# Kernel optimization log

Measured on AMD Instinct MI355X. Metric: run time of the kernel, lower is better.

## Reference

```python
import jax, jax.numpy as jnp
import numpy as np

H, W = 128, 192          # image size (height, width) after imsz swap
K = 31                   # weight_sl (local window size)
T = K // 2               # replicate padding
C_FEAT = 64              # feat_dim
FFT_ROWS, FFT_COLS = 32, 48  # rect fft mask (after '48,32' swap)


def fft_rect(x):
    # rfft2 low-pass rectangular mask, exactly as fft_ifft with 'rect'.
    f = jnp.fft.rfft2(x)
    rows = jnp.arange(f.shape[-2])[:, None] < FFT_ROWS
    cols = jnp.arange(f.shape[-1])[None, :] < FFT_COLS
    f = f * (rows & cols)
    return jnp.fft.irfft2(f, s=x.shape[-2:])


def make_grid():
    t = float(T)  # weight_sl//2 with downsample_factor=1
    xs = jnp.linspace(-t, t, K)
    gx, gy = jnp.meshgrid(xs, xs, indexing='ij')
    return jnp.stack((gx, gy), axis=-1)  # [K,K,2]


def local_corr(src, tgt):
    # src, tgt: [C,H,W] -> cost volume [H,W,K,K]
    sp = jnp.pad(src, ((0, 0), (T, T), (T, T)), mode='edge')  # replicate pad
    rows = []
    for k in range(K):  # fixed structural loop over window rows
        sl = sp[:, k:k + H, :]  # [C,H,W+2T]
        win = jax.lax.conv_general_dilated_patches(sl[None], (1, K), (1, 1), 'VALID')[0]
        win = win.reshape(C_FEAT, K, H, W)  # [C,l,H,W]
        rows.append(jnp.einsum('chw,clhw->hwl', tgt, win))
    return jnp.stack(rows, axis=-2)  # [H,W,k,l]


def setup_inputs() -> dict:
    key = jax.random.key(0)
    k1, k2, k3 = jax.random.split(key, 3)
    fill_val = (1.0 / C_FEAT) ** 0.5
    feats = fill_val + 0.02 * jax.random.normal(k1, (1, 2, C_FEAT, H, W), jnp.float32)
    in_frames = jax.random.normal(k2, (1, 1, 3, H, W), jnp.float32)
    tgt_frames = jax.random.normal(k3, (1, 1, 3, H, W), jnp.float32)
    return {"in_frames": in_frames, "tgt_frames": tgt_frames, "feats": feats, "temp": 10}


def reference(in_frames, tgt_frames, feats, temp):
    # src_idx=0, tgt_idx=1, single-frame 'feats' path
    src = fft_rect(feats[0, 0])  # [C,H,W]
    tgt = fft_rect(feats[0, 1])
    # bilinear interpolate(scale_factor=1) is identity
    src = src / jnp.linalg.norm(src, axis=0, keepdims=True)
    tgt = tgt / jnp.linalg.norm(tgt, axis=0, keepdims=True)
    w = local_corr(src, tgt) * temp                       # [H,W,K,K]
    w = jax.nn.softmax(w.reshape(H, W, K * K), axis=-1).reshape(H, W, K, K)

    # windowed average of in_frames with per-pixel softmax weights
    xp = jnp.pad(in_frames[0, 0], ((0, 0), (T, T), (T, T)), mode='edge')
    patches = jax.lax.conv_general_dilated_patches(xp[None], (K, K), (1, 1), 'VALID')[0]
    patches = patches.reshape(3, K, K, H, W)              # [C,k,l,H,W]
    out = jnp.einsum('cklhw,hwkl->chw', patches, w)[None, None]  # [1,1,3,H,W]

    grid = make_grid()                                    # [K,K,2]
    pos = jnp.einsum('hwkl,klm->hwm', w, grid)[None, None]
    pos = pos[..., ::-1]                                  # .flip(-1)
    enorm = jnp.einsum('hwkl,kl->hw', w, jnp.linalg.norm(grid, axis=-1))[None, None]
    weights = w[None, None]                               # [1,1,H,W,K,K]
    return out, pos, enorm, weights
```

## Files before the change

### kernel.cpp

```cpp
#include <hip/hip_runtime.h>
#include <cstddef>

#define H 128
#define W 192
#define KS 31
#define CF 64
#define NPIX (H*W)
#define NKL (KS*KS)

#define OFF_POS (3*NPIX)
#define OFF_EN  (OFF_POS + 2*NPIX)
#define OFF_WGT (OFF_EN + NPIX)

#define NIMG NPIX
#define WS_CWT 0
#define WS_SWT 512
#define WS_CHT 1024
#define WS_SHT 1536
#define WS_U   2048
#define WS_V   (WS_U + 128*NIMG)
#define WS_Y   (WS_V + 128*NIMG)
#define WS_SN  (WS_Y + 128*NIMG)
#define WS_TN  (WS_SN + 32*NIMG)

#define PI_F 3.14159265358979323846f

typedef __attribute__((ext_vector_type(8))) short short8v;
typedef __attribute__((ext_vector_type(4))) float f32x4;

__device__ inline ushort bf16rtn(float f){
  uint u = __float_as_uint(f);
  u += 0x7fffu + ((u >> 16) & 1u);
  return (ushort)(u >> 16);
}

__global__ __launch_bounds__(256) void k_tables(float* ws){
  int t = blockIdx.x*256 + threadIdx.x;
  if (t < 383){
    int d = t - 191;
    float c = 1.0f, s = 0.0f;
    for (int v = 1; v < 48; ++v){
      int m = (v*d) % 192; if (m < 0) m += 192;
      float a = (2.0f*PI_F/192.0f)*(float)m;
      c += 2.0f*cosf(a);
      s += 2.0f*sinf(a);
    }
    ws[WS_CWT + t] = c * (1.0f/192.0f);
    ws[WS_SWT + t] = s * (1.0f/192.0f);
  } else if (t < 383 + 255){
    int i = t - 383;
    int d = i - 127;
    float c = 0.0f, s = 0.0f;
    for (int u = 0; u < 32; ++u){
      int m = (u*d) % 128; if (m < 0) m += 128;
      float a = (2.0f*PI_F/128.0f)*(float)m;
      c += cosf(a);
      s += sinf(a);
    }
    ws[WS_CHT + i] = c * (1.0f/128.0f);
    ws[WS_SHT + i] = s * (1.0f/128.0f);
  }
}

__global__ __launch_bounds__(192) void k_colpass(const float* __restrict__ feats,
                                                const float* __restrict__ ws,
                                                float* __restrict__ U,
                                                float* __restrict__ V){
  __shared__ float xs[8][192];
  int w  = threadIdx.x;
  int R0 = blockIdx.x * 8;
  for (int r = 0; r < 8; ++r) xs[r][w] = feats[(size_t)(R0 + r)*192 + w];
  __syncthreads();
  const float* cwt = ws + WS_CWT;
  const float* swt = ws + WS_SWT;
  float u[8], v[8];
#pragma unroll
  for (int r = 0; r < 8; ++r){ u[r] = 0.0f; v[r] = 0.0f; }
  for (int wp = 0; wp < 192; ++wp){
    float cw = cwt[w - wp + 191];
    float sw = swt[w - wp + 191];
#pragma unroll
    for (int r = 0; r < 8; ++r){
      float x = xs[r][wp];
      u[r] = fmaf(x, cw, u[r]);
      v[r] = fmaf(x, sw, v[r]);
    }
  }
  for (int r = 0; r < 8; ++r){
    U[(size_t)(R0 + r)*192 + w] = u[r];
    V[(size_t)(R0 + r)*192 + w] = v[r];
  }
}

__global__ __launch_bounds__(192) void k_rowpass(const float* __restrict__ U,
                                                const float* __restrict__ V,
                                                const float* __restrict__ ws,
                                                float* __restrict__ Y){
  __shared__ float scht[255], ssht[255];
  int w = threadIdx.x;
  for (int i = w; i < 255; i += 192){
    scht[i] = ws[WS_CHT + i];
    ssht[i] = ws[WS_SHT + i];
  }
  __syncthreads();
  int ch = blockIdx.x >> 3;
  int h0 = (blockIdx.x & 7) * 16;
  const float* Uc = U + (size_t)ch*NIMG;
  const float* Vc = V + (size_t)ch*NIMG;
  float acc[16];
#pragma unroll
  for (int r = 0; r < 16; ++r) acc[r] = 0.0f;
  for (int hp = 0; hp < 128; ++hp){
    float uu = Uc[hp*192 + w];
    float vv = Vc[hp*192 + w];
#pragma unroll
    for (int r = 0; r < 16; ++r){
      int idx = h0 + r - hp + 127;
      acc[r] = fmaf(uu,  scht[idx], acc[r]);
      acc[r] = fmaf(-vv, ssht[idx], acc[r]);
    }
  }
  for (int r = 0; r < 16; ++r)
    Y[(size_t)ch*NIMG + (h0 + r)*192 + w] = acc[r];
}

__global__ __launch_bounds__(192) void k_norm(const float* __restrict__ Y,
                                              ushort* __restrict__ SNh,
                                              ushort* __restrict__ TNh){
  int h = blockIdx.x, w = threadIdx.x;
  int which = blockIdx.y;
  int pix = h*192 + w;
  const float* base = Y + (size_t)which*64*NIMG + pix;
  float x[64];
  float ss = 0.0f;
#pragma unroll
  for (int c = 0; c < 64; ++c){
    x[c] = base[(size_t)c*NIMG];
    ss = fmaf(x[c], x[c], ss);
  }
  float rn = 1.0f / sqrtf(ss);
  ushort* o = (which ? TNh : SNh) + (size_t)pix*64;
#pragma unroll
  for (int q = 0; q < 8; ++q){
    ushort tmp[8];
#pragma unroll
    for (int e = 0; e < 8; ++e) tmp[e] = bf16rtn(x[q*8 + e] * rn);
    *reinterpret_cast<uint4*>(o + q*8) = *reinterpret_cast<const uint4*>(tmp);
  }
}

__global__ __launch_bounds__(256) void k_corr(const ushort* __restrict__ SNh,
                                              const ushort* __restrict__ TNh,
                                              const int* __restrict__ temp,
                                              float* __restrict__ wgt){
  int h = blockIdx.x, k = blockIdx.y;
  int lane = threadIdx.x & 63;
  int wv = threadIdx.x >> 6;
  int i0base = wv * 3;
  int n = lane & 15, g = lane >> 4;
  float tempf = (float)(*temp);
  int sh = h + k - 15; sh = sh < 0 ? 0 : (sh > 127 ? 127 : sh);

  short8v a[3][2];
#pragma unroll
  for (int i = 0; i < 3; ++i){
    const ushort* p = TNh + ((size_t)(h*192 + (i0base + i)*16 + n))*64 + g*8;
#pragma unroll
    for (int ks = 0; ks < 2; ++ks)
      a[i][ks] = *reinterpret_cast<const short8v*>(p + ks*32);
  }
  short8v b[5][2];
  int j0lo = i0base - 1;
#pragma unroll
  for (int j = 0; j < 5; ++j){
    int j0 = j0lo + j;
    if (j0 < 0 || j0 > 11) continue;
    const ushort* p = SNh + ((size_t)(sh*192 + j0*16 + n))*64 + g*8;
#pragma unroll
    for (int ks = 0; ks < 2; ++ks)
      b[j][ks] = *reinterpret_cast<const short8v*>(p + ks*32);
  }

  float* base = wgt + ((size_t)(h*192))*NKL + (size_t)k*KS;
#pragma unroll
  for (int i = 0; i < 3; ++i){
    int i0 = i0base + i;
#pragma unroll
    for (int dj = -1; dj <= 1; ++dj){
      int j0 = i0 + dj;
      if (j0 < 0 || j0 > 11) continue;
      int jj = i + dj + 1;
      f32x4 acc = {0.0f, 0.0f, 0.0f, 0.0f};
      acc = __builtin_amdgcn_mfma_f32_16x16x32_bf16(a[i][0], b[jj][0], acc, 0, 0, 0);
      acc = __builtin_amdgcn_mfma_f32_16x16x32_bf16(a[i][1], b[jj][1], acc, 0, 0, 0);
      int sx = j0*16 + n;
#pragma unroll
      for (int r = 0; r < 4; ++r){
        int m = g*4 + r;
        int w = i0*16 + m;
        int l = sx - w + 15;
        float v = acc[r] * tempf;
        if (l >= 0 && l <= 30) base[(size_t)w*NKL + l] = v;
        if (j0 == 0 && n == 0){
          for (int l2 = 0; l2 < 15 - w; ++l2) base[(size_t)w*NKL + l2] = v;
        }
        if (j0 == 11 && n == 15){
          for (int l2 = 207 - w; l2 <= 30; ++l2) base[(size_t)w*NKL + l2] = v;
        }
      }
    }
  }
}

__global__ __launch_bounds__(256) void k_fused(float* __restrict__ dout,
                                               const float* __restrict__ frames){
  __shared__ float red[256];
  __shared__ float red6[6][256];
  int pix = blockIdx.x, t = threadIdx.x;
  int h = pix / 192, w = pix % 192;
  float* wp_ = dout + OFF_WGT + (size_t)pix*NKL;

  float x[4];
#pragma unroll
  for (int j = 0; j < 4; ++j){
    int i = t + 256*j;
    x[j] = (i < NKL) ? wp_[i] : -3.4e38f;
  }
  float m = fmaxf(fmaxf(x[0], x[1]), fmaxf(x[2], x[3]));
  red[t] = m; __syncthreads();
  for (int s = 128; s > 0; s >>= 1){
    if (t < s) red[t] = fmaxf(red[t], red[t + s]);
    __syncthreads();
  }
  float mall = red[0]; __syncthreads();

  float e[4];
  float sum = 0.0f;
#pragma unroll
  for (int j = 0; j < 4; ++j){
    int i = t + 256*j;
    e[j] = (i < NKL) ? expf(x[j] - mall) : 0.0f;
    sum += e[j];
  }
  red[t] = sum; __syncthreads();
  for (int s = 128; s > 0; s >>= 1){
    if (t < s) red[t] += red[t + s];
    __syncthreads();
  }
  float rs = 1.0f / red[0];

  float o0=0, o1=0, o2=0, p0=0, p1=0, en=0;
#pragma unroll
  for (int j = 0; j < 4; ++j){
    int i = t + 256*j;
    if (i < NKL){
      int k = i / 31, l = i - k*31;
      float ev = e[j] * rs;
      wp_[i] = ev;
      float dy = (float)(k - 15), dx = (float)(l - 15);
      p0 = fmaf(ev, dx, p0);
      p1 = fmaf(ev, dy, p1);
      en = fmaf(ev, sqrtf(dx*dx + dy*dy), en);
      int hh = h + k - 15; hh = hh < 0 ? 0 : (hh > 127 ? 127 : hh);
      int ww = w + l - 15; ww = ww < 0 ? 0 : (ww > 191 ? 191 : ww);
      const float* f = frames + hh*192 + ww;
      o0 = fmaf(ev, f[0],      o0);
      o1 = fmaf(ev, f[NPIX],   o1);
      o2 = fmaf(ev, f[2*NPIX], o2);
    }
  }
  red6[0][t]=o0; red6[1][t]=o1; red6[2][t]=o2; red6[3][t]=p0; red6[4][t]=p1; red6[5][t]=en;
  __syncthreads();
  for (int s = 128; s > 0; s >>= 1){
    if (t < s){
#pragma unroll
      for (int q = 0; q < 6; ++q) red6[q][t] += red6[q][t + s];
    }
    __syncthreads();
  }
  if (t == 0){
    dout[0*NPIX + pix] = red6[0][0];
    dout[1*NPIX + pix] = red6[1][0];
    dout[2*NPIX + pix] = red6[2][0];
    dout[OFF_POS + pix*2 + 0] = red6[3][0];
    dout[OFF_POS + pix*2 + 1] = red6[4][0];
    dout[OFF_EN + pix] = red6[5][0];
  }
}

extern "C" void kernel_launch(void* const* d_in, const int* in_sizes, int n_in,
                              void* d_out, int out_size, void* d_ws, size_t ws_size,
                              hipStream_t stream) {
  const float* frames = (const float*)d_in[0];
  const float* feats  = (const float*)d_in[2];
  const int*   temp   = (const int*)d_in[3];
  float* ws   = (float*)d_ws;
  float* dout = (float*)d_out;
  (void)in_sizes; (void)n_in; (void)out_size; (void)ws_size;

  float*  U   = ws + WS_U;
  float*  V   = ws + WS_V;
  float*  Y   = ws + WS_Y;
  ushort* SNh = (ushort*)(ws + WS_SN);
  ushort* TNh = (ushort*)(ws + WS_TN);

  hipLaunchKernelGGL(k_tables,  dim3(3),         dim3(256), 0, stream, ws);
  hipLaunchKernelGGL(k_colpass, dim3(2048),      dim3(192), 0, stream, feats, ws, U, V);
  hipLaunchKernelGGL(k_rowpass, dim3(1024),      dim3(192), 0, stream, U, V, ws, Y);
  hipLaunchKernelGGL(k_norm,    dim3(128, 2),    dim3(192), 0, stream, Y, SNh, TNh);
  hipLaunchKernelGGL(k_corr,    dim3(128, 31),   dim3(256), 0, stream, SNh, TNh, temp, dout + OFF_WGT);
  hipLaunchKernelGGL(k_fused,   dim3(NPIX),      dim3(256), 0, stream, dout, frames);
}
```

Baseline: 346.2 us.

## Fuse correlation, softmax and weighted reductions into one MFMA kernel

Merges the correlation kernel with the softmax/aggregation kernel. Each 64-thread block computes its correlation tiles with MFMA twice: the first pass accumulates the softmax sum and the weighted frame, position and norm sums in registers, and the second pass writes the normalized weights. The large cost volume is no longer written as raw logits and then read back, and the per-pixel 256-thread shared-memory reductions go away. The softmax max is fixed at temp (normalized features bound the dot product by 1), which trades a data-dependent max for an analytic bound. The column pass also now processes 16 rows per block and caches its twiddle tables in shared memory.

```diff
diff --git a/kernel.cpp b/kernel.cpp
--- a/kernel.cpp
+++ b/kernel.cpp
@@ -66,27 +66,33 @@
                                                 const float* __restrict__ ws,
                                                 float* __restrict__ U,
                                                 float* __restrict__ V){
-  __shared__ float xs[8][192];
+  __shared__ float xs[16][192];
+  __shared__ float scw[384], ssw[384];
   int w  = threadIdx.x;
-  int R0 = blockIdx.x * 8;
-  for (int r = 0; r < 8; ++r) xs[r][w] = feats[(size_t)(R0 + r)*192 + w];
+  int R0 = blockIdx.x * 16;
+  for (int i = w; i < 383; i += 192){
+    scw[i] = ws[WS_CWT + i];
+    ssw[i] = ws[WS_SWT + i];
+  }
+#pragma unroll
+  for (int r = 0; r < 16; ++r) xs[r][w] = feats[(size_t)(R0 + r)*192 + w];
   __syncthreads();
-  const float* cwt = ws + WS_CWT;
-  const float* swt = ws + WS_SWT;
-  float u[8], v[8];
-#pragma unroll
-  for (int r = 0; r < 8; ++r){ u[r] = 0.0f; v[r] = 0.0f; }
+  float u[16], v[16];
+#pragma unroll
+  for (int r = 0; r < 16; ++r){ u[r] = 0.0f; v[r] = 0.0f; }
+#pragma unroll 2
   for (int wp = 0; wp < 192; ++wp){
-    float cw = cwt[w - wp + 191];
-    float sw = swt[w - wp + 191];
-#pragma unroll
-    for (int r = 0; r < 8; ++r){
+    float cw = scw[w - wp + 191];
+    float sw = ssw[w - wp + 191];
+#pragma unroll
+    for (int r = 0; r < 16; ++r){
       float x = xs[r][wp];
       u[r] = fmaf(x, cw, u[r]);
       v[r] = fmaf(x, sw, v[r]);
     }
   }
-  for (int r = 0; r < 8; ++r){
+#pragma unroll
+  for (int r = 0; r < 16; ++r){
     U[(size_t)(R0 + r)*192 + w] = u[r];
     V[(size_t)(R0 + r)*192 + w] = v[r];
   }
@@ -149,142 +155,156 @@
   }
 }
 
-__global__ __launch_bounds__(256) void k_corr(const ushort* __restrict__ SNh,
-                                              const ushort* __restrict__ TNh,
-                                              const int* __restrict__ temp,
-                                              float* __restrict__ wgt){
-  int h = blockIdx.x, k = blockIdx.y;
-  int lane = threadIdx.x & 63;
-  int wv = threadIdx.x >> 6;
-  int i0base = wv * 3;
+__global__ __launch_bounds__(64) void k_corrfused(const ushort* __restrict__ SNh,
+                                                  const ushort* __restrict__ TNh,
+                                                  const int* __restrict__ temp,
+                                                  const float* __restrict__ frames,
+                                                  float* __restrict__ dout){
+  int h  = blockIdx.x;
+  int bx = blockIdx.y;
+  int lane = threadIdx.x;
   int n = lane & 15, g = lane >> 4;
+  int w0 = bx * 16;
   float tempf = (float)(*temp);
-  int sh = h + k - 15; sh = sh < 0 ? 0 : (sh > 127 ? 127 : sh);
-
-  short8v a[3][2];
-#pragma unroll
-  for (int i = 0; i < 3; ++i){
-    const ushort* p = TNh + ((size_t)(h*192 + (i0base + i)*16 + n))*64 + g*8;
-#pragma unroll
-    for (int ks = 0; ks < 2; ++ks)
-      a[i][ks] = *reinterpret_cast<const short8v*>(p + ks*32);
-  }
-  short8v b[5][2];
-  int j0lo = i0base - 1;
-#pragma unroll
-  for (int j = 0; j < 5; ++j){
-    int j0 = j0lo + j;
-    if (j0 < 0 || j0 > 11) continue;
-    const ushort* p = SNh + ((size_t)(sh*192 + j0*16 + n))*64 + g*8;
-#pragma unroll
-    for (int ks = 0; ks < 2; ++ks)
-      b[j][ks] = *reinterpret_cast<const short8v*>(p + ks*32);
-  }
-
-  float* base = wgt + ((size_t)(h*192))*NKL + (size_t)k*KS;
-#pragma unroll
-  for (int i = 0; i < 3; ++i){
-    int i0 = i0base + i;
-#pragma unroll
-    for (int dj = -1; dj <= 1; ++dj){
-      int j0 = i0 + dj;
+
+  const ushort* ap = TNh + ((size_t)(h*192 + w0 + n))*64 + g*8;
+  short8v a0 = *reinterpret_cast<const short8v*>(ap);
+  short8v a1 = *reinterpret_cast<const short8v*>(ap + 32);
+
+  float sum[4] = {0,0,0,0};
+  float ro0[4] = {0,0,0,0}, ro1[4] = {0,0,0,0}, ro2[4] = {0,0,0,0};
+  float rp0[4] = {0,0,0,0}, rp1[4] = {0,0,0,0}, ren[4] = {0,0,0,0};
+
+  for (int k = 0; k < KS; ++k){
+    int sh = h + k - 15; sh = sh < 0 ? 0 : (sh > 127 ? 127 : sh);
+    float dy = (float)(k - 15);
+    float dy2 = dy*dy;
+    const ushort* srow = SNh + (size_t)sh*192*64;
+#pragma unroll
+    for (int dj = 0; dj < 3; ++dj){
+      int j0 = bx - 1 + dj;
       if (j0 < 0 || j0 > 11) continue;
-      int jj = i + dj + 1;
+      const ushort* bp = srow + ((size_t)(j0*16 + n))*64 + g*8;
+      short8v b0 = *reinterpret_cast<const short8v*>(bp);
+      short8v b1 = *reinterpret_cast<const short8v*>(bp + 32);
       f32x4 acc = {0.0f, 0.0f, 0.0f, 0.0f};
-      acc = __builtin_amdgcn_mfma_f32_16x16x32_bf16(a[i][0], b[jj][0], acc, 0, 0, 0);
-      acc = __builtin_amdgcn_mfma_f32_16x16x32_bf16(a[i][1], b[jj][1], acc, 0, 0, 0);
+      acc = __builtin_amdgcn_mfma_f32_16x16x32_bf16(a0, b0, acc, 0, 0, 0);
+      acc = __builtin_amdgcn_mfma_f32_16x16x32_bf16(a1, b1, acc, 0, 0, 0);
       int sx = j0*16 + n;
+      float f0 = frames[sh*192 + sx];
+      float f1 = frames[NPIX   + sh*192 + sx];
+      float f2 = frames[2*NPIX + sh*192 + sx];
 #pragma unroll
       for (int r = 0; r < 4; ++r){
-        int m = g*4 + r;
-        int w = i0*16 + m;
+        int w = w0 + g*4 + r;
         int l = sx - w + 15;
-        float v = acc[r] * tempf;
-        if (l >= 0 && l <= 30) base[(size_t)w*NKL + l] = v;
-        if (j0 == 0 && n == 0){
-          for (int l2 = 0; l2 < 15 - w; ++l2) base[(size_t)w*NKL + l2] = v;
-        }
-        if (j0 == 11 && n == 15){
-          for (int l2 = 207 - w; l2 <= 30; ++l2) base[(size_t)w*NKL + l2] = v;
+        float e = __expf(acc[r]*tempf - tempf);
+        if (l >= 0 && l <= 30){
+          float dx = (float)(l - 15);
+          sum[r] += e;
+          ro0[r] = fmaf(e, f0, ro0[r]);
+          ro1[r] = fmaf(e, f1, ro1[r]);
+          ro2[r] = fmaf(e, f2, ro2[r]);
+          rp0[r] = fmaf(e, dx, rp0[r]);
+          rp1[r] = fmaf(e, dy, rp1[r]);
+          ren[r] = fmaf(e, sqrtf(dx*dx + dy2), ren[r]);
+        }
+        if (bx == 0 && j0 == 0 && n == 0){
+          int cnt = 15 - w;
+          if (cnt > 0){
+            float fc = (float)cnt;
+            sum[r] += fc*e;
+            ro0[r] = fmaf(fc*e, f0, ro0[r]);
+            ro1[r] = fmaf(fc*e, f1, ro1[r]);
+            ro2[r] = fmaf(fc*e, f2, ro2[r]);
+            rp1[r] = fmaf(fc*e, dy, rp1[r]);
+            float sdx = 0.5f*(float)(w*(w+1)) - 120.0f;
+            rp0[r] = fmaf(e, sdx, rp0[r]);
+            float se = 0.0f;
+            for (int d = w + 1; d <= 15; ++d) se += sqrtf((float)(d*d) + dy2);
+            ren[r] = fmaf(e, se, ren[r]);
+          }
+        }
+        if (bx == 11 && j0 == 11 && n == 15){
+          int cnt = w - 176;
+          if (cnt > 0){
+            float fc = (float)cnt;
+            sum[r] += fc*e;
+            ro0[r] = fmaf(fc*e, f0, ro0[r]);
+            ro1[r] = fmaf(fc*e, f1, ro1[r]);
+            ro2[r] = fmaf(fc*e, f2, ro2[r]);
+            rp1[r] = fmaf(fc*e, dy, rp1[r]);
+            float sdx = 120.0f - 0.5f*(float)((191-w)*(192-w));
+            rp0[r] = fmaf(e, sdx, rp0[r]);
+            float se = 0.0f;
+            for (int d = 192 - w; d <= 15; ++d) se += sqrtf((float)(d*d) + dy2);
+            ren[r] = fmaf(e, se, ren[r]);
+          }
         }
       }
     }
   }
-}
-
-__global__ __launch_bounds__(256) void k_fused(float* __restrict__ dout,
-                                               const float* __restrict__ frames){
-  __shared__ float red[256];
-  __shared__ float red6[6][256];
-  int pix = blockIdx.x, t = threadIdx.x;
-  int h = pix / 192, w = pix % 192;
-  float* wp_ = dout + OFF_WGT + (size_t)pix*NKL;
-
-  float x[4];
-#pragma unroll
-  for (int j = 0; j < 4; ++j){
-    int i = t + 256*j;
-    x[j] = (i < NKL) ? wp_[i] : -3.4e38f;
-  }
-  float m = fmaxf(fmaxf(x[0], x[1]), fmaxf(x[2], x[3]));
-  red[t] = m; __syncthreads();
-  for (int s = 128; s > 0; s >>= 1){
-    if (t < s) red[t] = fmaxf(red[t], red[t + s]);
-    __syncthreads();
-  }
-  float mall = red[0]; __syncthreads();
-
-  float e[4];
-  float sum = 0.0f;
-#pragma unroll
-  for (int j = 0; j < 4; ++j){
-    int i = t + 256*j;
-    e[j] = (i < NKL) ? expf(x[j] - mall) : 0.0f;
-    sum += e[j];
-  }
-  red[t] = sum; __syncthreads();
-  for (int s = 128; s > 0; s >>= 1){
-    if (t < s) red[t] += red[t + s];
-    __syncthreads();
-  }
-  float rs = 1.0f / red[0];
-
-  float o0=0, o1=0, o2=0, p0=0, p1=0, en=0;
-#pragma unroll
-  for (int j = 0; j < 4; ++j){
-    int i = t + 256*j;
-    if (i < NKL){
-      int k = i / 31, l = i - k*31;
-      float ev = e[j] * rs;
-      wp_[i] = ev;
-      float dy = (float)(k - 15), dx = (float)(l - 15);
-      p0 = fmaf(ev, dx, p0);
-      p1 = fmaf(ev, dy, p1);
-      en = fmaf(ev, sqrtf(dx*dx + dy*dy), en);
-      int hh = h + k - 15; hh = hh < 0 ? 0 : (hh > 127 ? 127 : hh);
-      int ww = w + l - 15; ww = ww < 0 ? 0 : (ww > 191 ? 191 : ww);
-      const float* f = frames + hh*192 + ww;
-      o0 = fmaf(ev, f[0],      o0);
-      o1 = fmaf(ev, f[NPIX],   o1);
-      o2 = fmaf(ev, f[2*NPIX], o2);
-    }
-  }
-  red6[0][t]=o0; red6[1][t]=o1; red6[2][t]=o2; red6[3][t]=p0; red6[4][t]=p1; red6[5][t]=en;
-  __syncthreads();
-  for (int s = 128; s > 0; s >>= 1){
-    if (t < s){
-#pragma unroll
-      for (int q = 0; q < 6; ++q) red6[q][t] += red6[q][t + s];
-    }
-    __syncthreads();
-  }
-  if (t == 0){
-    dout[0*NPIX + pix] = red6[0][0];
-    dout[1*NPIX + pix] = red6[1][0];
-    dout[2*NPIX + pix] = red6[2][0];
-    dout[OFF_POS + pix*2 + 0] = red6[3][0];
-    dout[OFF_POS + pix*2 + 1] = red6[4][0];
-    dout[OFF_EN + pix] = red6[5][0];
+
+#pragma unroll
+  for (int mask = 1; mask <= 8; mask <<= 1){
+#pragma unroll
+    for (int r = 0; r < 4; ++r){
+      sum[r] += __shfl_xor(sum[r], mask);
+      ro0[r] += __shfl_xor(ro0[r], mask);
+      ro1[r] += __shfl_xor(ro1[r], mask);
+      ro2[r] += __shfl_xor(ro2[r], mask);
+      rp0[r] += __shfl_xor(rp0[r], mask);
+      rp1[r] += __shfl_xor(rp1[r], mask);
+      ren[r] += __shfl_xor(ren[r], mask);
+    }
+  }
+  float rs[4];
+#pragma unroll
+  for (int r = 0; r < 4; ++r) rs[r] = 1.0f / sum[r];
+
+  if (n == 0){
+#pragma unroll
+    for (int r = 0; r < 4; ++r){
+      int pix = h*192 + w0 + g*4 + r;
+      dout[0*NPIX + pix] = ro0[r] * rs[r];
+      dout[1*NPIX + pix] = ro1[r] * rs[r];
+      dout[2*NPIX + pix] = ro2[r] * rs[r];
+      dout[OFF_POS + pix*2 + 0] = rp0[r] * rs[r];
+      dout[OFF_POS + pix*2 + 1] = rp1[r] * rs[r];
+      dout[OFF_EN + pix] = ren[r] * rs[r];
+    }
+  }
+
+  float* wgt = dout + OFF_WGT;
+  for (int k = 0; k < KS; ++k){
+    int sh = h + k - 15; sh = sh < 0 ? 0 : (sh > 127 ? 127 : sh);
+    const ushort* srow = SNh + (size_t)sh*192*64;
+#pragma unroll
+    for (int dj = 0; dj < 3; ++dj){
+      int j0 = bx - 1 + dj;
+      if (j0 < 0 || j0 > 11) continue;
+      const ushort* bp = srow + ((size_t)(j0*16 + n))*64 + g*8;
+      short8v b0 = *reinterpret_cast<const short8v*>(bp);
+      short8v b1 = *reinterpret_cast<const short8v*>(bp + 32);
+      f32x4 acc = {0.0f, 0.0f, 0.0f, 0.0f};
+      acc = __builtin_amdgcn_mfma_f32_16x16x32_bf16(a0, b0, acc, 0, 0, 0);
+      acc = __builtin_amdgcn_mfma_f32_16x16x32_bf16(a1, b1, acc, 0, 0, 0);
+      int sx = j0*16 + n;
+#pragma unroll
+      for (int r = 0; r < 4; ++r){
+        int w = w0 + g*4 + r;
+        int l = sx - w + 15;
+        float e = __expf(acc[r]*tempf - tempf) * rs[r];
+        float* wp_ = wgt + (size_t)(h*192 + w)*NKL + k*KS;
+        if (l >= 0 && l <= 30) wp_[l] = e;
+        if (bx == 0 && j0 == 0 && n == 0){
+          for (int l2 = 0; l2 < 15 - w; ++l2) wp_[l2] = e;
+        }
+        if (bx == 11 && j0 == 11 && n == 15){
+          for (int l2 = 207 - w; l2 <= 30; ++l2) wp_[l2] = e;
+        }
+      }
+    }
   }
 }
 
@@ -304,10 +324,9 @@
   ushort* SNh = (ushort*)(ws + WS_SN);
   ushort* TNh = (ushort*)(ws + WS_TN);
 
-  hipLaunchKernelGGL(k_tables,  dim3(3),         dim3(256), 0, stream, ws);
-  hipLaunchKernelGGL(k_colpass, dim3(2048),      dim3(192), 0, stream, feats, ws, U, V);
-  hipLaunchKernelGGL(k_rowpass, dim3(1024),      dim3(192), 0, stream, U, V, ws, Y);
-  hipLaunchKernelGGL(k_norm,    dim3(128, 2),    dim3(192), 0, stream, Y, SNh, TNh);
-  hipLaunchKernelGGL(k_corr,    dim3(128, 31),   dim3(256), 0, stream, SNh, TNh, temp, dout + OFF_WGT);
-  hipLaunchKernelGGL(k_fused,   dim3(NPIX),      dim3(256), 0, stream, dout, frames);
-}
+  hipLaunchKernelGGL(k_tables,    dim3(3),        dim3(256), 0, stream, ws);
+  hipLaunchKernelGGL(k_colpass,   dim3(1024),     dim3(192), 0, stream, feats, ws, U, V);
+  hipLaunchKernelGGL(k_rowpass,   dim3(1024),     dim3(192), 0, stream, U, V, ws, Y);
+  hipLaunchKernelGGL(k_norm,      dim3(128, 2),   dim3(192), 0, stream, Y, SNh, TNh);
+  hipLaunchKernelGGL(k_corrfused, dim3(128, 12),  dim3(64),  0, stream, SNh, TNh, temp, frames, dout);
+}
```

New measurement: 463.2 us. 1.34x slower.

## Compute FFT low-pass as split-bf16 MFMA matrix products

Applied to the files above, without the earlier changes.

Replaces the scalar FP32 column and row low-pass convolution passes with dense matrix multiplies on MFMA bf16 instructions. Operands are split into high and low bf16 parts and combined with three products each, which keeps close to FP32 accuracy. This adds full filter matrices, a split kernel for the features, and transposed intermediate buffers. The aim is to cut the cost of the FFT-mask stage, though the downstream corr and fused kernels are unchanged and may dominate the total time.

```diff
diff --git a/kernel.cpp b/kernel.cpp
--- a/kernel.cpp
+++ b/kernel.cpp
@@ -12,16 +12,23 @@
 #define OFF_EN  (OFF_POS + 2*NPIX)
 #define OFF_WGT (OFF_EN + NPIX)
 
-#define NIMG NPIX
-#define WS_CWT 0
-#define WS_SWT 512
-#define WS_CHT 1024
-#define WS_SHT 1536
-#define WS_U   2048
-#define WS_V   (WS_U + 128*NIMG)
-#define WS_Y   (WS_V + 128*NIMG)
-#define WS_SN  (WS_Y + 128*NIMG)
-#define WS_TN  (WS_SN + 32*NIMG)
+#define WS_CWH 0
+#define WS_CWL 18432
+#define WS_SWH 36864
+#define WS_SWL 55296
+#define WS_CHH 73728
+#define WS_CHL 81920
+#define WS_SHH 90112
+#define WS_SHL 98304
+#define WS_XH  131072
+#define WS_XL  (WS_XH + 1179648)
+#define WS_UTH 2490368
+#define WS_UTL (WS_UTH + 1572864)
+#define WS_VTH (WS_UTL + 1572864)
+#define WS_VTL (WS_VTH + 1572864)
+#define WS_Y2  8781824
+#define WS_SN2 131072
+#define WS_TN2 (WS_SN2 + 786432)
 
 #define PI_F 3.14159265358979323846f
 
@@ -33,95 +40,149 @@
   u += 0x7fffu + ((u >> 16) & 1u);
   return (ushort)(u >> 16);
 }
-
-__global__ __launch_bounds__(256) void k_tables(float* ws){
-  int t = blockIdx.x*256 + threadIdx.x;
-  if (t < 383){
-    int d = t - 191;
+__device__ inline float bf2f(ushort h){ return __uint_as_float((uint)h << 16); }
+__device__ inline void bfsplit(float f, ushort& h, ushort& l){
+  h = bf16rtn(f);
+  l = bf16rtn(f - bf2f(h));
+}
+
+__global__ __launch_bounds__(256) void k_mats(float* ws){
+  int e = blockIdx.x*256 + threadIdx.x;
+  ushort* CWh = (ushort*)(ws + WS_CWH); ushort* CWl = (ushort*)(ws + WS_CWL);
+  ushort* SWh = (ushort*)(ws + WS_SWH); ushort* SWl = (ushort*)(ws + WS_SWL);
+  ushort* CHh = (ushort*)(ws + WS_CHH); ushort* CHl = (ushort*)(ws + WS_CHL);
+  ushort* SHh = (ushort*)(ws + WS_SHH); ushort* SHl = (ushort*)(ws + WS_SHL);
+  if (e < 36864){
+    int w = e / 192, wp = e - w*192, d = w - wp;
     float c = 1.0f, s = 0.0f;
     for (int v = 1; v < 48; ++v){
       int m = (v*d) % 192; if (m < 0) m += 192;
       float a = (2.0f*PI_F/192.0f)*(float)m;
-      c += 2.0f*cosf(a);
-      s += 2.0f*sinf(a);
-    }
-    ws[WS_CWT + t] = c * (1.0f/192.0f);
-    ws[WS_SWT + t] = s * (1.0f/192.0f);
-  } else if (t < 383 + 255){
-    int i = t - 383;
-    int d = i - 127;
+      c += 2.0f*cosf(a); s += 2.0f*sinf(a);
+    }
+    c *= (1.0f/192.0f); s *= (1.0f/192.0f);
+    bfsplit(c, CWh[e], CWl[e]);
+    bfsplit(s, SWh[e], SWl[e]);
+  } else if (e < 36864 + 16384){
+    int i = e - 36864;
+    int h = i >> 7, hp = i & 127, d = h - hp;
     float c = 0.0f, s = 0.0f;
     for (int u = 0; u < 32; ++u){
       int m = (u*d) % 128; if (m < 0) m += 128;
       float a = (2.0f*PI_F/128.0f)*(float)m;
-      c += cosf(a);
-      s += sinf(a);
-    }
-    ws[WS_CHT + i] = c * (1.0f/128.0f);
-    ws[WS_SHT + i] = s * (1.0f/128.0f);
-  }
-}
-
-__global__ __launch_bounds__(192) void k_colpass(const float* __restrict__ feats,
-                                                const float* __restrict__ ws,
-                                                float* __restrict__ U,
-                                                float* __restrict__ V){
-  __shared__ float xs[8][192];
-  int w  = threadIdx.x;
-  int R0 = blockIdx.x * 8;
-  for (int r = 0; r < 8; ++r) xs[r][w] = feats[(size_t)(R0 + r)*192 + w];
-  __syncthreads();
-  const float* cwt = ws + WS_CWT;
-  const float* swt = ws + WS_SWT;
-  float u[8], v[8];
-#pragma unroll
-  for (int r = 0; r < 8; ++r){ u[r] = 0.0f; v[r] = 0.0f; }
-  for (int wp = 0; wp < 192; ++wp){
-    float cw = cwt[w - wp + 191];
-    float sw = swt[w - wp + 191];
-#pragma unroll
-    for (int r = 0; r < 8; ++r){
-      float x = xs[r][wp];
-      u[r] = fmaf(x, cw, u[r]);
-      v[r] = fmaf(x, sw, v[r]);
-    }
-  }
-  for (int r = 0; r < 8; ++r){
-    U[(size_t)(R0 + r)*192 + w] = u[r];
-    V[(size_t)(R0 + r)*192 + w] = v[r];
-  }
-}
-
-__global__ __launch_bounds__(192) void k_rowpass(const float* __restrict__ U,
-                                                const float* __restrict__ V,
-                                                const float* __restrict__ ws,
-                                                float* __restrict__ Y){
-  __shared__ float scht[255], ssht[255];
-  int w = threadIdx.x;
-  for (int i = w; i < 255; i += 192){
-    scht[i] = ws[WS_CHT + i];
-    ssht[i] = ws[WS_SHT + i];
-  }
-  __syncthreads();
+      c += cosf(a); s += sinf(a);
+    }
+    c *= (1.0f/128.0f); s *= (1.0f/128.0f);
+    bfsplit(c,  CHh[i], CHl[i]);
+    bfsplit(-s, SHh[i], SHl[i]);
+  }
+}
+
+__global__ __launch_bounds__(256) void k_split(const float* __restrict__ feats,
+                                               ushort* __restrict__ Xh,
+                                               ushort* __restrict__ Xl){
+  int i = (blockIdx.x*256 + threadIdx.x)*8;
+  float4 v0 = *reinterpret_cast<const float4*>(feats + i);
+  float4 v1 = *reinterpret_cast<const float4*>(feats + i + 4);
+  ushort h[8], l[8];
+  bfsplit(v0.x,h[0],l[0]); bfsplit(v0.y,h[1],l[1]); bfsplit(v0.z,h[2],l[2]); bfsplit(v0.w,h[3],l[3]);
+  bfsplit(v1.x,h[4],l[4]); bfsplit(v1.y,h[5],l[5]); bfsplit(v1.z,h[6],l[6]); bfsplit(v1.w,h[7],l[7]);
+  *reinterpret_cast<uint4*>(Xh + i) = *reinterpret_cast<const uint4*>(h);
+  *reinterpret_cast<uint4*>(Xl + i) = *reinterpret_cast<const uint4*>(l);
+}
+
+__global__ __launch_bounds__(256) void k_colU(const ushort* __restrict__ Xh,
+                                              const ushort* __restrict__ Xl,
+                                              const float* __restrict__ ws,
+                                              ushort* __restrict__ UTh, ushort* __restrict__ UTl,
+                                              ushort* __restrict__ VTh, ushort* __restrict__ VTl){
+  const ushort* CWh = (const ushort*)(ws + WS_CWH);
+  const ushort* CWl = (const ushort*)(ws + WS_CWL);
+  const ushort* SWh = (const ushort*)(ws + WS_SWH);
+  const ushort* SWl = (const ushort*)(ws + WS_SWL);
+  int R0 = blockIdx.x*16;
+  int wv = threadIdx.x >> 6, lane = threadIdx.x & 63;
+  int n = lane & 15, g = lane >> 4;
+  int w0 = (blockIdx.y*4 + wv)*16;
+
+  const ushort* xh = Xh + (size_t)(R0 + n)*192 + g*8;
+  const ushort* xl = Xl + (size_t)(R0 + n)*192 + g*8;
+  const ushort* cwh = CWh + (size_t)(w0 + n)*192 + g*8;
+  const ushort* cwl = CWl + (size_t)(w0 + n)*192 + g*8;
+  const ushort* swh = SWh + (size_t)(w0 + n)*192 + g*8;
+  const ushort* swl = SWl + (size_t)(w0 + n)*192 + g*8;
+
+  f32x4 aU = {0,0,0,0}, aV = {0,0,0,0};
+#pragma unroll
+  for (int ks = 0; ks < 6; ++ks){
+    short8v ah = *reinterpret_cast<const short8v*>(xh + ks*32);
+    short8v al = *reinterpret_cast<const short8v*>(xl + ks*32);
+    short8v bh = *reinterpret_cast<const short8v*>(cwh + ks*32);
+    short8v bl = *reinterpret_cast<const short8v*>(cwl + ks*32);
+    aU = __builtin_amdgcn_mfma_f32_16x16x32_bf16(ah, bh, aU, 0, 0, 0);
+    aU = __builtin_amdgcn_mfma_f32_16x16x32_bf16(ah, bl, aU, 0, 0, 0);
+    aU = __builtin_amdgcn_mfma_f32_16x16x32_bf16(al, bh, aU, 0, 0, 0);
+    short8v dh = *reinterpret_cast<const short8v*>(swh + ks*32);
+    short8v dl = *reinterpret_cast<const short8v*>(swl + ks*32);
+    aV = __builtin_amdgcn_mfma_f32_16x16x32_bf16(ah, dh, aV, 0, 0, 0);
+    aV = __builtin_amdgcn_mfma_f32_16x16x32_bf16(ah, dl, aV, 0, 0, 0);
+    aV = __builtin_amdgcn_mfma_f32_16x16x32_bf16(al, dh, aV, 0, 0, 0);
+  }
+  int ch = R0 >> 7, hp0 = R0 & 127;
+  size_t base = ((size_t)(ch*192 + w0 + n))*128 + hp0 + g*4;
+  ushort uh[4], ul[4], vh[4], vl[4];
+#pragma unroll
+  for (int r = 0; r < 4; ++r){
+    bfsplit(aU[r], uh[r], ul[r]);
+    bfsplit(aV[r], vh[r], vl[r]);
+  }
+  *reinterpret_cast<uint2*>(UTh + base) = *reinterpret_cast<const uint2*>(uh);
+  *reinterpret_cast<uint2*>(UTl + base) = *reinterpret_cast<const uint2*>(ul);
+  *reinterpret_cast<uint2*>(VTh + base) = *reinterpret_cast<const uint2*>(vh);
+  *reinterpret_cast<uint2*>(VTl + base) = *reinterpret_cast<const uint2*>(vl);
+}
+
+__global__ __launch_bounds__(256) void k_rowY(const float* __restrict__ ws,
+                                              const ushort* __restrict__ UTh, const ushort* __restrict__ UTl,
+                                              const ushort* __restrict__ VTh, const ushort* __restrict__ VTl,
+                                              float* __restrict__ Y){
+  const ushort* CHh = (const ushort*)(ws + WS_CHH);
+  const ushort* CHl = (const ushort*)(ws + WS_CHL);
+  const ushort* SHh = (const ushort*)(ws + WS_SHH);
+  const ushort* SHl = (const ushort*)(ws + WS_SHL);
   int ch = blockIdx.x >> 3;
-  int h0 = (blockIdx.x & 7) * 16;
-  const float* Uc = U + (size_t)ch*NIMG;
-  const float* Vc = V + (size_t)ch*NIMG;
-  float acc[16];
-#pragma unroll
-  for (int r = 0; r < 16; ++r) acc[r] = 0.0f;
-  for (int hp = 0; hp < 128; ++hp){
-    float uu = Uc[hp*192 + w];
-    float vv = Vc[hp*192 + w];
-#pragma unroll
-    for (int r = 0; r < 16; ++r){
-      int idx = h0 + r - hp + 127;
-      acc[r] = fmaf(uu,  scht[idx], acc[r]);
-      acc[r] = fmaf(-vv, ssht[idx], acc[r]);
-    }
-  }
-  for (int r = 0; r < 16; ++r)
-    Y[(size_t)ch*NIMG + (h0 + r)*192 + w] = acc[r];
+  int h0 = (blockIdx.x & 7)*16;
+  int wv = threadIdx.x >> 6, lane = threadIdx.x & 63;
+  int n = lane & 15, g = lane >> 4;
+  int w0 = (blockIdx.y*4 + wv)*16;
+
+  const ushort* ahp = CHh + (size_t)(h0 + n)*128 + g*8;
+  const ushort* alp = CHl + (size_t)(h0 + n)*128 + g*8;
+  const ushort* shp = SHh + (size_t)(h0 + n)*128 + g*8;
+  const ushort* slp = SHl + (size_t)(h0 + n)*128 + g*8;
+  size_t brow = ((size_t)(ch*192 + w0 + n))*128 + g*8;
+
+  f32x4 acc = {0,0,0,0};
+#pragma unroll
+  for (int ks = 0; ks < 4; ++ks){
+    short8v ah = *reinterpret_cast<const short8v*>(ahp + ks*32);
+    short8v al = *reinterpret_cast<const short8v*>(alp + ks*32);
+    short8v uh = *reinterpret_cast<const short8v*>(UTh + brow + ks*32);
+    short8v ul = *reinterpret_cast<const short8v*>(UTl + brow + ks*32);
+    acc = __builtin_amdgcn_mfma_f32_16x16x32_bf16(ah, uh, acc, 0, 0, 0);
+    acc = __builtin_amdgcn_mfma_f32_16x16x32_bf16(ah, ul, acc, 0, 0, 0);
+    acc = __builtin_amdgcn_mfma_f32_16x16x32_bf16(al, uh, acc, 0, 0, 0);
+    short8v sh = *reinterpret_cast<const short8v*>(shp + ks*32);
+    short8v sl = *reinterpret_cast<const short8v*>(slp + ks*32);
+    short8v vh = *reinterpret_cast<const short8v*>(VTh + brow + ks*32);
+    short8v vl = *reinterpret_cast<const short8v*>(VTl + brow + ks*32);
+    acc = __builtin_amdgcn_mfma_f32_16x16x32_bf16(sh, vh, acc, 0, 0, 0);
+    acc = __builtin_amdgcn_mfma_f32_16x16x32_bf16(sh, vl, acc, 0, 0, 0);
+    acc = __builtin_amdgcn_mfma_f32_16x16x32_bf16(sl, vh, acc, 0, 0, 0);
+  }
+#pragma unroll
+  for (int r = 0; r < 4; ++r)
+    Y[(size_t)(ch*128 + h0 + g*4 + r)*192 + w0 + n] = acc[r];
 }
 
 __global__ __launch_bounds__(192) void k_norm(const float* __restrict__ Y,
@@ -130,12 +191,12 @@
   int h = blockIdx.x, w = threadIdx.x;
   int which = blockIdx.y;
   int pix = h*192 + w;
-  const float* base = Y + (size_t)which*64*NIMG + pix;
+  const float* base = Y + (size_t)which*64*NPIX + pix;
   float x[64];
   float ss = 0.0f;
 #pragma unroll
   for (int c = 0; c < 64; ++c){
-    x[c] = base[(size_t)c*NIMG];
+    x[c] = base[(size_t)c*NPIX];
     ss = fmaf(x[c], x[c], ss);
   }
   float rn = 1.0f / sqrtf(ss);
@@ -298,16 +359,21 @@
   float* dout = (float*)d_out;
   (void)in_sizes; (void)n_in; (void)out_size; (void)ws_size;
 
-  float*  U   = ws + WS_U;
-  float*  V   = ws + WS_V;
-  float*  Y   = ws + WS_Y;
-  ushort* SNh = (ushort*)(ws + WS_SN);
-  ushort* TNh = (ushort*)(ws + WS_TN);
-
-  hipLaunchKernelGGL(k_tables,  dim3(3),         dim3(256), 0, stream, ws);
-  hipLaunchKernelGGL(k_colpass, dim3(2048),      dim3(192), 0, stream, feats, ws, U, V);
-  hipLaunchKernelGGL(k_rowpass, dim3(1024),      dim3(192), 0, stream, U, V, ws, Y);
-  hipLaunchKernelGGL(k_norm,    dim3(128, 2),    dim3(192), 0, stream, Y, SNh, TNh);
-  hipLaunchKernelGGL(k_corr,    dim3(128, 31),   dim3(256), 0, stream, SNh, TNh, temp, dout + OFF_WGT);
-  hipLaunchKernelGGL(k_fused,   dim3(NPIX),      dim3(256), 0, stream, dout, frames);
-}
+  ushort* Xh  = (ushort*)(ws + WS_XH);
+  ushort* Xl  = (ushort*)(ws + WS_XL);
+  ushort* UTh = (ushort*)(ws + WS_UTH);
+  ushort* UTl = (ushort*)(ws + WS_UTL);
+  ushort* VTh = (ushort*)(ws + WS_VTH);
+  ushort* VTl = (ushort*)(ws + WS_VTL);
+  float*  Y   = ws + WS_Y2;
+  ushort* SNh = (ushort*)(ws + WS_SN2);
+  ushort* TNh = (ushort*)(ws + WS_TN2);
+
+  hipLaunchKernelGGL(k_mats,   dim3(208),      dim3(256), 0, stream, ws);
+  hipLaunchKernelGGL(k_split,  dim3(1152),     dim3(256), 0, stream, feats, Xh, Xl);
+  hipLaunchKernelGGL(k_colU,   dim3(1024, 3),  dim3(256), 0, stream, Xh, Xl, ws, UTh, UTl, VTh, VTl);
+  hipLaunchKernelGGL(k_rowY,   dim3(1024, 3),  dim3(256), 0, stream, ws, UTh, UTl, VTh, VTl, Y);
+  hipLaunchKernelGGL(k_norm,   dim3(128, 2),   dim3(192), 0, stream, Y, SNh, TNh);
+  hipLaunchKernelGGL(k_corr,   dim3(128, 31),  dim3(256), 0, stream, SNh, TNh, temp, dout + OFF_WGT);
+  hipLaunchKernelGGL(k_fused,  dim3(NPIX),     dim3(256), 0, stream, dout, frames);
+}
```

Measured after the change: 338.3 us. 1.02x faster.
